# Kernel tuning notes

Measured on AMD Instinct MI355X. Metric: run time of the kernel, lower is better.

Reference implementation:

```python
import jax, jax.numpy as jnp
import numpy as np

D_IN = 2048
D_OUT = 2048
SEQ = 4096


def setup_inputs() -> dict:
    key = jax.random.key(0)
    kx, kq, kk, kv = jax.random.split(key, 4)
    x = jax.random.normal(kx, (SEQ, D_IN), dtype=jnp.float32)
    # torch.nn.Linear weights have shape [d_out, d_in]
    s = 1.0 / np.sqrt(D_IN)
    W_q = jax.random.uniform(kq, (D_OUT, D_IN), jnp.float32, -s, s)
    W_k = jax.random.uniform(kk, (D_OUT, D_IN), jnp.float32, -s, s)
    W_v = jax.random.uniform(kv, (D_OUT, D_IN), jnp.float32, -s, s)
    return {"x": x, "W_q": W_q, "W_k": W_k, "W_v": W_v}


def reference(x, W_q, W_k, W_v):
    # projections (torch Linear: x @ W.T)
    q = x @ W_q.T  # [S, D]
    k = x @ W_k.T
    v = x @ W_v.T
    scores = q @ k.T  # [S, S]
    scale = jnp.asarray(k.shape[-1], scores.dtype) ** 0.5
    attn = jax.nn.softmax(scores / scale, axis=-1)
    # post-softmax causal mask + row renormalization (faithful to source)
    S = scores.shape[0]
    mask = jnp.tril(jnp.ones((S, S), dtype=attn.dtype))
    masked = attn * mask
    masked = masked / masked.sum(axis=1, keepdims=True)
    return masked @ v  # [S, D]
```

## Files before the change

kernel.cpp:

```cpp
#include <hip/hip_runtime.h>
#include <hip/hip_bf16.h>
#include <math.h>


typedef __attribute__((ext_vector_type(8))) short bf16x8;
typedef __attribute__((ext_vector_type(4))) float f32x4;
typedef __attribute__((ext_vector_type(8))) unsigned short u16x8;
typedef __attribute__((ext_vector_type(4))) int iv4;

__device__ __forceinline__ unsigned short f2bf(float f) {
  unsigned int u = __float_as_uint(f);
  u += 0x7FFFu + ((u >> 16) & 1u);
  return (unsigned short)(u >> 16);
}
__device__ __forceinline__ float bf2f(unsigned short u) {
  return __uint_as_float((unsigned int)u << 16);
}

__device__ __forceinline__ void gload16(const unsigned short* g, unsigned short* l) {
  __builtin_amdgcn_global_load_lds(
      (const __attribute__((address_space(1))) void*)g,
      (__attribute__((address_space(3))) void*)l,
      16, 0, 0);
}

template <int OFF>
__device__ __forceinline__ bf16x8 dsr(unsigned addr) {
  iv4 r;
  asm volatile("ds_read_b128 %0, %1 offset:%2" : "=v"(r) : "v"(addr), "i"(OFF));
  return __builtin_bit_cast(bf16x8, r);
}

__global__ void cvt_all(const float* __restrict__ x, const float* __restrict__ wq,
                        const float* __restrict__ wk, const float* __restrict__ wv,
                        unsigned short* __restrict__ xb, unsigned short* __restrict__ wqb,
                        unsigned short* __restrict__ wkb, unsigned short* __restrict__ wvb) {
  const int SD = 4096 * 2048, DD = 2048 * 2048;
  int i = (blockIdx.x * 256 + threadIdx.x) * 8;
  const float* in;
  unsigned short* out;
  int off;
  if (i < SD)               { in = x;  out = xb;  off = i; }
  else if (i < SD + DD)     { in = wq; out = wqb; off = i - SD; }
  else if (i < SD + 2 * DD) { in = wk; out = wkb; off = i - SD - DD; }
  else                      { in = wv; out = wvb; off = i - SD - 2 * DD; }
  float4 a = *(const float4*)(in + off);
  float4 b = *(const float4*)(in + off + 4);
  u16x8 r;
  r[0] = f2bf(a.x); r[1] = f2bf(a.y); r[2] = f2bf(a.z); r[3] = f2bf(a.w);
  r[4] = f2bf(b.x); r[5] = f2bf(b.y); r[6] = f2bf(b.z); r[7] = f2bf(b.w);
  *(u16x8*)(out + off) = r;
}

#define LGKM_SB()                                         \
  asm volatile("s_waitcnt lgkmcnt(0)" ::: "memory");      \
  __builtin_amdgcn_sched_barrier(0)

#define QMFMA(MB, NB, AF, BV)                                                 \
  _Pragma("unroll")                                                           \
  for (int _fm = 0; _fm < 4; ++_fm)                                           \
    _Pragma("unroll")                                                         \
    for (int _fn = 0; _fn < 2; ++_fn)                                         \
      _Pragma("unroll")                                                       \
      for (int _ks = 0; _ks < 2; ++_ks)                                       \
        acc[(MB) + _fm][(NB) + _fn] = __builtin_amdgcn_mfma_f32_16x16x32_bf16( \
            AF[_fm * 2 + _ks], BV[_fn * 2 + _ks], acc[(MB) + _fm][(NB) + _fn], \
            0, 0, 0);

#define STG_A(mhv, tau, bufv)                                                 \
  do {                                                                        \
    unsigned short* _d = lds + (bufv) * 32768 + (mhv) * 8192 + w * 512;       \
    gload16(pA + (size_t)((mhv) * 64) * KC + ((size_t)(tau) << 6), _d);       \
    gload16(pA + (size_t)(128 + (mhv) * 64) * KC + ((size_t)(tau) << 6),      \
            _d + 4096);                                                       \
  } while (0)

#define STG_B(nhv, tau, bufv)                                                 \
  do {                                                                        \
    unsigned short* _d = lds + (bufv) * 32768 + 16384 + (nhv) * 8192 + w * 512;\
    gload16(pB + (size_t)((nhv) * 32) * KC + ((size_t)(tau) << 6), _d);       \
    gload16(pB + (size_t)(128 + (nhv) * 32) * KC + ((size_t)(tau) << 6),      \
            _d + 4096);                                                       \
  } while (0)

template <int KC>
__device__ __forceinline__ void gemm_core(const unsigned short* __restrict__ Ab,
                                          const unsigned short* __restrict__ Bb,
                                          unsigned short* lds, int ktiles,
                                          f32x4 (&acc)[8][4]) {
  const int tid  = threadIdx.x;
  const int lane = tid & 63;
  const int w    = tid >> 6;
  const int wm   = w >> 2;
  const int wn   = w & 3;

  const int base  = w * 8 + (lane >> 3);
  const int gslot = (lane & 7) ^ ((lane >> 3) & 7);
  const unsigned short* pA = Ab + (size_t)base * KC + gslot * 8;
  const unsigned short* pB =
      Bb + (size_t)((base >> 5) * 64 + (base & 31)) * KC + gslot * 8;

  const unsigned lb = (unsigned)(size_t)&lds[0];
  const int rl = lane & 15, g = lane >> 4;
  const unsigned sw0 = (unsigned)(((0 + g) ^ (rl & 7)) * 16);
  const unsigned sw1 = (unsigned)(((4 + g) ^ (rl & 7)) * 16);
  const unsigned rA = lb + (unsigned)(wm * 8192 + rl * 128);
  const unsigned rB = lb + (unsigned)(wn * 4096 + rl * 128);

#pragma unroll
  for (int m = 0; m < 8; ++m)
#pragma unroll
    for (int n = 0; n < 4; ++n) acc[m][n] = f32x4{0.f, 0.f, 0.f, 0.f};

  STG_A(0, 0, 0); STG_B(0, 0, 0); STG_A(1, 0, 0); STG_B(1, 0, 0);
  if (ktiles > 1) {
    STG_A(0, 1, 1); STG_B(0, 1, 1); STG_A(1, 1, 1);
    asm volatile("s_waitcnt vmcnt(6)" ::: "memory");
  } else {
    asm volatile("s_waitcnt vmcnt(0)" ::: "memory");
  }
  __builtin_amdgcn_s_barrier();

  bf16x8 af0[8], af1[8], bv0[4], bv1[4];
  {
    const unsigned aA0 = rA + sw0, aA1 = rA + sw1;
    const unsigned aB0 = rB + sw0, aB1 = rB + sw1;
    af0[0] = dsr<0>(aA0);     af0[1] = dsr<0>(aA1);
    af0[2] = dsr<2048>(aA0);  af0[3] = dsr<2048>(aA1);
    af0[4] = dsr<4096>(aA0);  af0[5] = dsr<4096>(aA1);
    af0[6] = dsr<6144>(aA0);  af0[7] = dsr<6144>(aA1);
    bv0[0] = dsr<32768>(aB0); bv0[1] = dsr<32768>(aB1);
    bv0[2] = dsr<34816>(aB0); bv0[3] = dsr<34816>(aB1);
  }

  for (int t = 0; t < ktiles; ++t) {
    const unsigned bo  = (unsigned)(t & 1) << 16;
    const unsigned bon = (unsigned)((t + 1) & 1) << 16;
    const int buf = t & 1, nb = (t + 1) & 1;
    const bool s1 = (t + 1) < ktiles, s2 = (t + 2) < ktiles;
    const bool tail = t >= ktiles - 2;
    const unsigned aA0 = rA + bo + sw0, aA1 = rA + bo + sw1;
    const unsigned aB0 = rB + bo + sw0, aB1 = rB + bo + sw1;
    const unsigned nA0 = rA + bon + sw0, nA1 = rA + bon + sw1;
    const unsigned nB0 = rB + bon + sw0, nB1 = rB + bon + sw1;

    LGKM_SB();
    af1[0] = dsr<16384>(aA0); af1[1] = dsr<16384>(aA1);
    af1[2] = dsr<18432>(aA0); af1[3] = dsr<18432>(aA1);
    af1[4] = dsr<20480>(aA0); af1[5] = dsr<20480>(aA1);
    af1[6] = dsr<22528>(aA0); af1[7] = dsr<22528>(aA1);
    bv1[0] = dsr<49152>(aB0); bv1[1] = dsr<49152>(aB1);
    bv1[2] = dsr<51200>(aB0); bv1[3] = dsr<51200>(aB1);
    __builtin_amdgcn_sched_barrier(0);
    __builtin_amdgcn_s_setprio(1);
    QMFMA(0, 0, af0, bv0);
    __builtin_amdgcn_s_setprio(0);
    LGKM_SB();
    __builtin_amdgcn_s_setprio(1);
    QMFMA(4, 0, af1, bv0);
    __builtin_amdgcn_s_setprio(0);
    if (s1) STG_B(1, t + 1, nb);
    if (s2) { STG_A(0, t + 2, buf); STG_B(0, t + 2, buf); }
    if (tail) { asm volatile("s_waitcnt vmcnt(0)" ::: "memory"); }
    else      { asm volatile("s_waitcnt vmcnt(8)" ::: "memory"); }
    __builtin_amdgcn_s_barrier();

    __builtin_amdgcn_sched_barrier(0);
    __builtin_amdgcn_s_setprio(1);
    QMFMA(0, 2, af0, bv1);
    __builtin_amdgcn_s_setprio(0);
    if (s1) {
      af0[0] = dsr<0>(nA0);     af0[1] = dsr<0>(nA1);
      af0[2] = dsr<2048>(nA0);  af0[3] = dsr<2048>(nA1);
      af0[4] = dsr<4096>(nA0);  af0[5] = dsr<4096>(nA1);
      af0[6] = dsr<6144>(nA0);  af0[7] = dsr<6144>(nA1);
      bv0[0] = dsr<32768>(nB0); bv0[1] = dsr<32768>(nB1);
      bv0[2] = dsr<34816>(nB0); bv0[3] = dsr<34816>(nB1);
    }
    __builtin_amdgcn_sched_barrier(0);
    __builtin_amdgcn_s_setprio(1);
    QMFMA(4, 2, af1, bv1);
    __builtin_amdgcn_s_setprio(0);
    if (s2) STG_A(1, t + 2, buf);
    if (tail) { asm volatile("s_waitcnt vmcnt(0)" ::: "memory"); }
    else      { asm volatile("s_waitcnt vmcnt(6)" ::: "memory"); }
    __builtin_amdgcn_s_barrier();
  }
}

__device__ __forceinline__ void ep_f32(float* C, const f32x4 (&acc)[8][4],
                                       int r0, int c0, int ldc, float scale) {
  const int lane = threadIdx.x & 63, w = threadIdx.x >> 6;
  const int crow0 = r0 + (w >> 2) * 128 + ((lane >> 4) << 2);
  const int ccol0 = c0 + (w & 3) * 64 + (lane & 15);
#pragma unroll
  for (int m = 0; m < 8; ++m)
#pragma unroll
    for (int n = 0; n < 4; ++n)
#pragma unroll
      for (int j = 0; j < 4; ++j)
        C[(size_t)(crow0 + m * 16 + j) * ldc + (ccol0 + n * 16)] =
            acc[m][n][j] * scale;
}

__device__ __forceinline__ void ep_f32_at(float* C, const f32x4 (&acc)[8][4],
                                          int r0, int c0, int ldc, float scale) {
  const int lane = threadIdx.x & 63, w = threadIdx.x >> 6;
  const int crow0 = r0 + (w >> 2) * 128 + ((lane >> 4) << 2);
  const int ccol0 = c0 + (w & 3) * 64 + (lane & 15);
#pragma unroll
  for (int m = 0; m < 8; ++m)
#pragma unroll
    for (int n = 0; n < 4; ++n)
#pragma unroll
      for (int j = 0; j < 4; ++j)
        atomicAdd(&C[(size_t)(crow0 + m * 16 + j) * ldc + (ccol0 + n * 16)],
                  acc[m][n][j] * scale);
}

__device__ __forceinline__ void ep_bf16(unsigned short* C, const f32x4 (&acc)[8][4],
                                        int r0, int c0, int ldc) {
  const int lane = threadIdx.x & 63, w = threadIdx.x >> 6;
  const int crow0 = r0 + (w >> 2) * 128 + ((lane >> 4) << 2);
  const int ccol0 = c0 + (w & 3) * 64 + (lane & 15);
#pragma unroll
  for (int m = 0; m < 8; ++m)
#pragma unroll
    for (int n = 0; n < 4; ++n)
#pragma unroll
      for (int j = 0; j < 4; ++j)
        C[(size_t)(crow0 + m * 16 + j) * ldc + (ccol0 + n * 16)] =
            f2bf(acc[m][n][j]);
}

__global__ __launch_bounds__(512, 2)
void proj_qk(const unsigned short* __restrict__ xb,
             const unsigned short* __restrict__ wqb,
             const unsigned short* __restrict__ wkb,
             unsigned short* __restrict__ Q, unsigned short* __restrict__ Kb) {
  __shared__ __align__(16) unsigned short lds[65536];
  const int bid = blockIdx.x;
  const int wg = (bid & 7) * 32 + (bid >> 3);
  const int bm = wg >> 4, bnr = wg & 15;
  const unsigned short* B = (bnr < 8) ? wqb : wkb;
  unsigned short* C = (bnr < 8) ? Q : Kb;
  const int bnl = bnr & 7;
  f32x4 acc[8][4];
  gemm_core<2048>(xb + (size_t)bm * 256 * 2048, B + (size_t)bnl * 256 * 2048,
                  lds, 32, acc);
  ep_bf16(C, acc, bm * 256, bnl * 256, 2048);
}

__global__ __launch_bounds__(512, 2)
void vt_qkt(const unsigned short* __restrict__ Qp,
            const unsigned short* __restrict__ Kp,
            const unsigned short* __restrict__ wvb,
            const unsigned short* __restrict__ xb,
            float* __restrict__ sc, unsigned short* __restrict__ Vt,
            float scale) {
  __shared__ __align__(16) unsigned short lds[65536];
  const int id = blockIdx.x;
  f32x4 acc[8][4];
  if (id < 64) {
    const int p = id >> 2, c = id & 3;
    const size_t koff = (size_t)c * 8 * 64;
    gemm_core<2048>(Qp + (size_t)15 * 256 * 2048 + koff,
                    Kp + (size_t)p * 256 * 2048 + koff, lds, 8, acc);
    ep_f32_at(sc, acc, 3840, p * 256, 4096, scale);
  } else if (id < 184) {
    const int q = id - 64;
    int bm = 0;
    while ((bm + 1) * (bm + 2) / 2 <= q) ++bm;
    const int bn = q - bm * (bm + 1) / 2;
    gemm_core<2048>(Qp + (size_t)bm * 256 * 2048,
                    Kp + (size_t)bn * 256 * 2048, lds, 32, acc);
    ep_f32(sc, acc, bm * 256, bn * 256, 4096, scale);
  } else {
    const int v = id - 184, bm = v >> 4, bn = v & 15;
    gemm_core<2048>(wvb + (size_t)bm * 256 * 2048,
                    xb + (size_t)bn * 256 * 2048, lds, 32, acc);
    ep_bf16(Vt, acc, bm * 256, bn * 256, 4096);
  }
}

__global__ __launch_bounds__(512, 2)
void pv_q(const unsigned short* __restrict__ P,
          const unsigned short* __restrict__ Vt, float* __restrict__ out,
          unsigned short* __restrict__ aux1, unsigned short* __restrict__ aux2,
          unsigned short* __restrict__ aux3, int* __restrict__ ctr) {
  __shared__ __align__(16) unsigned short lds[65536];
  __shared__ int sid;
  f32x4 acc[8][4];
  for (;;) {
    if (threadIdx.x == 0) sid = atomicAdd(ctr, 1);
    __syncthreads();
    const int id = sid;
    if (id >= 320) return;
    int rem = id, bm = 15, s = 4;
    for (;;) {
      s = (bm >> 2) + 1;
      const int cnt = 8 * s;
      if (rem < cnt) break;
      rem -= cnt;
      --bm;
    }
    const int bn = rem / s, p = rem % s;
    const int kt = (bm + 1) * 4;
    const int k0 = (kt * p) / s, k1 = (kt * (p + 1)) / s;
    gemm_core<4096>(P + (size_t)bm * 256 * 4096 + (size_t)k0 * 64,
                    Vt + (size_t)bn * 256 * 4096 + (size_t)k0 * 64,
                    lds, k1 - k0, acc);
    if (p == 0)      ep_f32(out,   acc, bm * 256,        bn * 256, 2048, 1.0f);
    else if (p == 1) ep_bf16(aux1, acc, bm * 256 - 1024, bn * 256, 2048);
    else if (p == 2) ep_bf16(aux2, acc, bm * 256 - 2048, bn * 256, 2048);
    else             ep_bf16(aux3, acc, bm * 256 - 3072, bn * 256, 2048);
  }
}

__global__ void add3(float* __restrict__ out, const unsigned short* __restrict__ aux1,
                     const unsigned short* __restrict__ aux2,
                     const unsigned short* __restrict__ aux3) {
  const size_t i = ((size_t)blockIdx.x * 256 + threadIdx.x) * 8;
  const int row = 1024 + (int)(i >> 11);
  float* o = out + (size_t)1024 * 2048 + i;
  f32x4 a0 = *(const f32x4*)o;
  f32x4 a1 = *(const f32x4*)(o + 4);
  u16x8 b = *(const u16x8*)(aux1 + i);
#pragma unroll
  for (int k = 0; k < 4; ++k) { a0[k] += bf2f(b[k]); a1[k] += bf2f(b[k + 4]); }
  if (row >= 2048) {
    const size_t j = i - (size_t)1024 * 2048;
    u16x8 c = *(const u16x8*)(aux2 + j);
#pragma unroll
    for (int k = 0; k < 4; ++k) { a0[k] += bf2f(c[k]); a1[k] += bf2f(c[k + 4]); }
  }
  if (row >= 3072) {
    const size_t j = i - (size_t)2048 * 2048;
    u16x8 d = *(const u16x8*)(aux3 + j);
#pragma unroll
    for (int k = 0; k < 4; ++k) { a0[k] += bf2f(d[k]); a1[k] += bf2f(d[k + 4]); }
  }
  *(f32x4*)o = a0;
  *(f32x4*)(o + 4) = a1;
}

__global__ void softmax_causal(const float* __restrict__ Sc,
                               unsigned short* __restrict__ P, int S) {
  const int i = blockIdx.x;
  const int tid = threadIdx.x;
  const int nvalid = i + 1;
  const int pad_end = ((i >> 8) + 1) << 8;
  const float* row = Sc + (size_t)i * S;

  float v[16];
  float m = -1e30f;
#pragma unroll
  for (int it = 0; it < 16; ++it) {
    const int j = tid + it * 256;
    const float x = (j < nvalid) ? row[j] : -1e30f;
    v[it] = x;
    m = fmaxf(m, x);
  }
#pragma unroll
  for (int d = 1; d < 64; d <<= 1) m = fmaxf(m, __shfl_xor(m, d));
  __shared__ float red_m[4], red_s[4];
  const int lane = tid & 63, wv = tid >> 6;
  if (lane == 0) red_m[wv] = m;
  __syncthreads();
  m = fmaxf(fmaxf(red_m[0], red_m[1]), fmaxf(red_m[2], red_m[3]));

  float s = 0.0f;
#pragma unroll
  for (int it = 0; it < 16; ++it) {
    const int j = tid + it * 256;
    const float e = (j < nvalid) ? __expf(v[it] - m) : 0.0f;
    v[it] = e;
    s += e;
  }
#pragma unroll
  for (int d = 1; d < 64; d <<= 1) s += __shfl_xor(s, d);
  if (lane == 0) red_s[wv] = s;
  __syncthreads();
  s = red_s[0] + red_s[1] + red_s[2] + red_s[3];

  const float inv = 1.0f / s;
  unsigned short* prow = P + (size_t)i * S;
#pragma unroll
  for (int it = 0; it < 16; ++it) {
    const int j = tid + it * 256;
    if (j < pad_end) prow[j] = (j < nvalid) ? f2bf(v[it] * inv) : (unsigned short)0;
  }
}

extern "C" void kernel_launch(void* const* d_in, const int* in_sizes, int n_in,
                              void* d_out, int out_size, void* d_ws, size_t ws_size,
                              hipStream_t stream) {
  const float* x  = (const float*)d_in[0];
  const float* Wq = (const float*)d_in[1];
  const float* Wk = (const float*)d_in[2];
  const float* Wv = (const float*)d_in[3];
  float* out = (float*)d_out;

  const int S = 4096, D = 2048;
  char* ws = (char*)d_ws;
  const size_t MB = 1u << 20;
  float*          sc   = (float*)ws;
  unsigned short* aux1 = (unsigned short*)ws;
  unsigned short* aux2 = (unsigned short*)(ws + 16 * MB);
  unsigned short* aux3 = (unsigned short*)(ws + 28 * MB);
  unsigned short* xb   = (unsigned short*)(ws + 64 * MB);
  unsigned short* wqb  = (unsigned short*)(ws + 80 * MB);
  unsigned short* wkb  = (unsigned short*)(ws + 88 * MB);
  unsigned short* wvb  = (unsigned short*)(ws + 96 * MB);
  unsigned short* Q    = (unsigned short*)(ws + 104 * MB);
  unsigned short* Kb   = (unsigned short*)(ws + 120 * MB);
  unsigned short* Vt   = (unsigned short*)(ws + 80 * MB);
  unsigned short* P    = (unsigned short*)(ws + 104 * MB);
  int*            ctr  = (int*)(ws + 136 * MB);

  cvt_all<<<(S * D + 3 * D * D) / (256 * 8), 256, 0, stream>>>(
      x, Wq, Wk, Wv, xb, wqb, wkb, wvb);

  hipMemsetAsync(ctr, 0, 16, stream);
  hipMemsetAsync(sc + (size_t)3840 * 4096, 0, (size_t)256 * 4096 * 4, stream);

  proj_qk<<<256, 512, 0, stream>>>(xb, wqb, wkb, Q, Kb);

  const float scale = 1.0f / sqrtf((float)D);
  vt_qkt<<<312, 512, 0, stream>>>(Q, Kb, wvb, xb, sc, Vt, scale);

  softmax_causal<<<S, 256, 0, stream>>>(sc, P, S);

  pv_q<<<256, 512, 0, stream>>>(P, Vt, out, aux1, aux2, aux3, ctr);
  add3<<<3072, 256, 0, stream>>>(out, aux1, aux2, aux3);
}
```

Before: 237.6 us.

## Restructure GEMM main loop into barrier-separated quarter-tile phases

Rewrites the K-loop schedule. Register fragments are no longer prefetched across iterations. Each iteration now loads its own fragments in four phases, with an s_barrier between each LDS read, global-to-LDS stage and MFMA group. The goal is to interleave the staging loads more evenly with the MFMA work and to keep register pressure down, at the cost of many more workgroup barriers and no overlap of the next tile's LDS reads with the current MFMAs. The ktiles==1 guard in the prologue is also dropped, and the tail waitcnt logic changes.

```diff
diff --git a/kernel.cpp b/kernel.cpp
--- a/kernel.cpp
+++ b/kernel.cpp
@@ -113,77 +113,57 @@
     for (int n = 0; n < 4; ++n) acc[m][n] = f32x4{0.f, 0.f, 0.f, 0.f};
 
   STG_A(0, 0, 0); STG_B(0, 0, 0); STG_A(1, 0, 0); STG_B(1, 0, 0);
-  if (ktiles > 1) {
-    STG_A(0, 1, 1); STG_B(0, 1, 1); STG_A(1, 1, 1);
-    asm volatile("s_waitcnt vmcnt(6)" ::: "memory");
-  } else {
-    asm volatile("s_waitcnt vmcnt(0)" ::: "memory");
-  }
+  STG_A(0, 1, 1); STG_B(0, 1, 1); STG_A(1, 1, 1);
+  asm volatile("s_waitcnt vmcnt(6)" ::: "memory");
   __builtin_amdgcn_s_barrier();
 
-  bf16x8 af0[8], af1[8], bv0[4], bv1[4];
-  {
-    const unsigned aA0 = rA + sw0, aA1 = rA + sw1;
-    const unsigned aB0 = rB + sw0, aB1 = rB + sw1;
+  for (int t = 0; t < ktiles; ++t) {
+    const unsigned bo = (unsigned)(t & 1) << 16;
+    const int buf = t & 1, nb = (t + 1) & 1;
+    const unsigned aA0 = rA + bo + sw0, aA1 = rA + bo + sw1;
+    const unsigned aB0 = rB + bo + sw0, aB1 = rB + bo + sw1;
+    bf16x8 af0[8], af1[8], bv0[4], bv1[4];
     af0[0] = dsr<0>(aA0);     af0[1] = dsr<0>(aA1);
     af0[2] = dsr<2048>(aA0);  af0[3] = dsr<2048>(aA1);
     af0[4] = dsr<4096>(aA0);  af0[5] = dsr<4096>(aA1);
     af0[6] = dsr<6144>(aA0);  af0[7] = dsr<6144>(aA1);
     bv0[0] = dsr<32768>(aB0); bv0[1] = dsr<32768>(aB1);
     bv0[2] = dsr<34816>(aB0); bv0[3] = dsr<34816>(aB1);
-  }
-
-  for (int t = 0; t < ktiles; ++t) {
-    const unsigned bo  = (unsigned)(t & 1) << 16;
-    const unsigned bon = (unsigned)((t + 1) & 1) << 16;
-    const int buf = t & 1, nb = (t + 1) & 1;
-    const bool s1 = (t + 1) < ktiles, s2 = (t + 2) < ktiles;
-    const bool tail = t >= ktiles - 2;
-    const unsigned aA0 = rA + bo + sw0, aA1 = rA + bo + sw1;
-    const unsigned aB0 = rB + bo + sw0, aB1 = rB + bo + sw1;
-    const unsigned nA0 = rA + bon + sw0, nA1 = rA + bon + sw1;
-    const unsigned nB0 = rB + bon + sw0, nB1 = rB + bon + sw1;
-
+    if (t + 1 < ktiles) STG_B(1, t + 1, nb);
+    __builtin_amdgcn_s_barrier();
     LGKM_SB();
+    __builtin_amdgcn_s_setprio(1);
+    QMFMA(0, 0, af0, bv0);
+    __builtin_amdgcn_s_setprio(0);
+    __builtin_amdgcn_s_barrier();
     af1[0] = dsr<16384>(aA0); af1[1] = dsr<16384>(aA1);
     af1[2] = dsr<18432>(aA0); af1[3] = dsr<18432>(aA1);
     af1[4] = dsr<20480>(aA0); af1[5] = dsr<20480>(aA1);
     af1[6] = dsr<22528>(aA0); af1[7] = dsr<22528>(aA1);
-    bv1[0] = dsr<49152>(aB0); bv1[1] = dsr<49152>(aB1);
-    bv1[2] = dsr<51200>(aB0); bv1[3] = dsr<51200>(aB1);
-    __builtin_amdgcn_sched_barrier(0);
-    __builtin_amdgcn_s_setprio(1);
-    QMFMA(0, 0, af0, bv0);
-    __builtin_amdgcn_s_setprio(0);
+    if (t + 2 < ktiles) STG_A(0, t + 2, buf);
+    __builtin_amdgcn_s_barrier();
     LGKM_SB();
     __builtin_amdgcn_s_setprio(1);
     QMFMA(4, 0, af1, bv0);
     __builtin_amdgcn_s_setprio(0);
-    if (s1) STG_B(1, t + 1, nb);
-    if (s2) { STG_A(0, t + 2, buf); STG_B(0, t + 2, buf); }
-    if (tail) { asm volatile("s_waitcnt vmcnt(0)" ::: "memory"); }
-    else      { asm volatile("s_waitcnt vmcnt(8)" ::: "memory"); }
-    __builtin_amdgcn_s_barrier();
-
-    __builtin_amdgcn_sched_barrier(0);
+    __builtin_amdgcn_s_barrier();
+    bv1[0] = dsr<49152>(aB0); bv1[1] = dsr<49152>(aB1);
+    bv1[2] = dsr<51200>(aB0); bv1[3] = dsr<51200>(aB1);
+    if (t + 2 < ktiles) STG_B(0, t + 2, buf);
+    __builtin_amdgcn_s_barrier();
+    LGKM_SB();
     __builtin_amdgcn_s_setprio(1);
     QMFMA(0, 2, af0, bv1);
     __builtin_amdgcn_s_setprio(0);
-    if (s1) {
-      af0[0] = dsr<0>(nA0);     af0[1] = dsr<0>(nA1);
-      af0[2] = dsr<2048>(nA0);  af0[3] = dsr<2048>(nA1);
-      af0[4] = dsr<4096>(nA0);  af0[5] = dsr<4096>(nA1);
-      af0[6] = dsr<6144>(nA0);  af0[7] = dsr<6144>(nA1);
-      bv0[0] = dsr<32768>(nB0); bv0[1] = dsr<32768>(nB1);
-      bv0[2] = dsr<34816>(nB0); bv0[3] = dsr<34816>(nB1);
-    }
-    __builtin_amdgcn_sched_barrier(0);
+    __builtin_amdgcn_s_barrier();
+    if (t + 2 < ktiles) STG_A(1, t + 2, buf);
+    __builtin_amdgcn_s_barrier();
+    LGKM_SB();
     __builtin_amdgcn_s_setprio(1);
     QMFMA(4, 2, af1, bv1);
     __builtin_amdgcn_s_setprio(0);
-    if (s2) STG_A(1, t + 2, buf);
-    if (tail) { asm volatile("s_waitcnt vmcnt(0)" ::: "memory"); }
-    else      { asm volatile("s_waitcnt vmcnt(6)" ::: "memory"); }
+    if (t < ktiles - 2)       { asm volatile("s_waitcnt vmcnt(6)" ::: "memory"); }
+    else if (t == ktiles - 2) { asm volatile("s_waitcnt vmcnt(0)" ::: "memory"); }
     __builtin_amdgcn_s_barrier();
   }
 }
```

Measured after the change: 244.5 us. 2.9% more time.
